# Optimization experiments

Hardware: AMD Instinct MI355X
Metric: run time of the kernel (lower is better)

## Reference

```python
import jax, jax.numpy as jnp
import numpy as np

HDIM = 1024
CDIM = 256
TEMPER = 10.0
IGNORE_OUT = 0.0
EPS = 1e-6


def setup_inputs() -> dict:
    key = jax.random.key(0)
    ks = jax.random.split(key, 6)
    B, T, D = 2, 128, 384
    x = jax.random.normal(ks[0], (B, T, D), jnp.float32)
    y = jax.random.normal(ks[1], (B, T, D), jnp.float32)
    # xavier-normal style init for the two linear layers
    W_enc = jax.random.normal(ks[2], (D, HDIM), jnp.float32) * np.sqrt(2.0 / (D + HDIM))
    b_enc = jnp.zeros((HDIM,), jnp.float32)
    W_dec = jax.random.normal(ks[3], (HDIM, D), jnp.float32) * np.sqrt(2.0 / (D + HDIM))
    b_dec = jnp.zeros((D,), jnp.float32)
    return {"x": x, "y": y, "W_enc": W_enc, "b_enc": b_enc, "W_dec": W_dec, "b_dec": b_dec}


def reference(x, y, W_enc, b_enc, W_dec, b_dec):
    B, T, D = x.shape
    n_iter = HDIM // CDIM
    pad = D - 1
    # shift_idx[s, j] = s + j : window of width D at offset s, s in [0, 2D-2]
    shift_idx = jnp.arange(2 * D - 1)[:, None] + jnp.arange(D)[None, :]

    seq_mask = (y == IGNORE_OUT)                       # (B,T,D) bool
    denom_seq = jnp.sum(~seq_mask).astype(x.dtype)
    qn = jnp.linalg.norm(y, axis=-1)                   # (B,T)

    mask_prev = None
    x_dis, losses = [], []
    for _ in range(n_iter):
        # --- _pad_for_shift: (B,T,2D-1,D) shifted windows of x ---
        kp = jnp.pad(x, ((0, 0), (0, 0), (pad, pad)))  # (B,T,3D-2)
        kpt = kp[..., shift_idx]                       # (B,T,2D-1,D)
        # --- _score (cos) + argmax over shifts ---
        kn = jnp.linalg.norm(kpt, axis=-1)             # (B,T,2D-1)
        sim = jnp.einsum('btsd,btd->bts', kpt, y) / (qn[..., None] * kn + EPS)
        sim = jnp.where(jnp.isnan(sim), 0.0, sim)
        theta = jnp.argmax(sim, axis=-1)               # (B,T) int
        x_opt = jnp.take_along_axis(kpt, theta[..., None, None], axis=-2)[..., 0, :]  # (B,T,D)
        # --- attention: elementwise cos-scaled score, temp softmax, detached ---
        dn = (jnp.linalg.norm(x_opt, axis=-1, keepdims=True)
              * jnp.linalg.norm(y, axis=-1, keepdims=True) + EPS)
        attn = jax.nn.softmax((x_opt * y / dn) / TEMPER, axis=-1)
        attn = jnp.where(jnp.isnan(attn), 0.0, attn)
        attn = jax.lax.stop_gradient(attn)
        x_attn = x_opt * attn
        # --- _reverse_pad_for_shift: window at offset 2D-2-theta ---
        kp2 = jnp.pad(x_attn, ((0, 0), (0, 0), (pad, pad)))
        rev_idx = (2 * D - 2 - theta)[..., None] + jnp.arange(D)  # (B,T,D)
        x_ele = jnp.take_along_axis(kp2, rev_idx, axis=-1)         # (B,T,D)
        # --- self_net: encoder -> top-k sparsify -> decoder_self ---
        h = x_ele @ W_enc + b_enc                      # (B,T,HDIM)
        if mask_prev is not None:
            h = jnp.where(mask_prev > 0, 1e-10, h)
        _, idx_top = jax.lax.top_k(h, CDIM)            # (B,T,CDIM)
        flat = idx_top.reshape(B * T, CDIM)
        mask_cur = jnp.zeros((B * T, HDIM), x.dtype).at[
            jnp.arange(B * T)[:, None], flat].set(1.0).reshape(B, T, HDIM)
        if mask_prev is None:
            mask_prev = mask_cur
        else:
            mask_prev = mask_prev + mask_cur - mask_prev * mask_cur
        h = h * mask_cur
        out = h @ W_dec + b_dec                        # (B,T,D)
        x_dis.append(out)
        # --- SeqLoss (masked MSE, mean-reduced by count of valid elems) ---
        err = jnp.where(seq_mask, 0.0, (out - x) ** 2) / denom_seq
        losses.append(jnp.sum(err))
    return jnp.stack(x_dis), jnp.stack(losses)
```

## Files before the change

### kernel.cpp

```cpp
#include <hip/hip_runtime.h>
#include <hip/hip_fp16.h>
#include <math.h>

#define DD 384
#define HD 1024
#define CD 256
#define NS 765
#define NITER 4
#define NROWS 256
#define TEMPER_F 10.0f
#define EPSF 1e-6f
#define CUTF 1e-10f

typedef unsigned long long u64;
typedef unsigned int u32;
typedef _Float16 hh2 __attribute__((ext_vector_type(2)));

__device__ __forceinline__ u32 flipf(float f) {
    u32 u = __float_as_uint(f);
    return u ^ ((u32)((int)u >> 31) | 0x80000000u);
}
__device__ __forceinline__ u32 bf16r(float f) {
    u32 u = __float_as_uint(f);
    return (u + 0x7FFFu + ((u >> 16) & 1u)) >> 16;
}
__device__ __forceinline__ u32 pack2bf(float a, float b) {
    return bf16r(a) | (bf16r(b) << 16);
}
__device__ __forceinline__ float blo(u32 p) { return __uint_as_float(p << 16); }
__device__ __forceinline__ float bhi(u32 p) { return __uint_as_float(p & 0xFFFF0000u); }
__device__ __forceinline__ u32 packh2(float a, float b) {
    __half2 p = __floats2half2_rn(a, b);
    return __builtin_bit_cast(u32, p);
}
__device__ __forceinline__ float dot2(u32 a, u32 b, float c) {
#if __has_builtin(__builtin_amdgcn_fdot2)
    return __builtin_amdgcn_fdot2(__builtin_bit_cast(hh2, a),
                                  __builtin_bit_cast(hh2, b), c, false);
#else
    __half2 ah = __builtin_bit_cast(__half2, a);
    __half2 bh = __builtin_bit_cast(__half2, b);
    return fmaf(__half2float(ah.y), __half2float(bh.y),
           fmaf(__half2float(ah.x), __half2float(bh.x), c));
#endif
}

__global__ __launch_bounds__(256) void convert_kernel(
    const float* __restrict__ We, const float* __restrict__ Wd,
    u32* __restrict__ wencp, uint2* __restrict__ wd16)
{
    const int t = blockIdx.x * 256 + threadIdx.x;
    for (int i = t; i < 192 * HD; i += 65536) {
        int j2 = i >> 10, c = i & 1023;
        wencp[i] = packh2(We[(2 * j2) * HD + c], We[(2 * j2 + 1) * HD + c]);
    }
    for (int i = t; i < (HD * DD) / 4; i += 65536) {
        float4 v = ((const float4*)Wd)[i];
        wd16[i] = make_uint2(pack2bf(v.x, v.y), pack2bf(v.z, v.w));
    }
}

__global__ __launch_bounds__(1024) void fused_kernel(
    const float* __restrict__ x, const float* __restrict__ y,
    const u32* __restrict__ wencp, const float* __restrict__ benc,
    const u32* __restrict__ wdec16, const float* __restrict__ bdec,
    float* __restrict__ out_xdis, float* __restrict__ lossp,
    int* __restrict__ ycnt)
{
    const int row  = blockIdx.x;
    const int tid  = threadIdx.x;
    const int lane = tid & 63;
    const int wid  = tid >> 6;

    __shared__ __align__(16) float xpad[1152];
    __shared__ __align__(16) float yr[DD];
    __shared__ float xa[DD];
    __shared__ __align__(16) float xe_s[DD];
    __shared__ u32   xep[192];
    __shared__ __align__(16) float part[4][HD];
    __shared__ u32   sk0[HD], sk1[HD];
    __shared__ __align__(16) uint2 dec2[HD];
    __shared__ __align__(16) float4 dpart[8][96];
    __shared__ float wred[16];
    __shared__ int   wredi[16];
    __shared__ float wredn[16];
    __shared__ float s_sc[4];
    __shared__ int   s_theta;
    __shared__ u32   s_b1, s_b2, s_b3;
    __shared__ int   wcls[128];
    __shared__ int   sbase[128];
    __shared__ int   cnt8[8];
    __shared__ float loss4[NITER];

    const float* xrow = x + row * DD;
    const float* yrow = y + row * DD;

    for (int i = tid; i < 1152; i += 1024)
        xpad[i] = (i >= DD - 1 && i < 2 * DD - 1) ? xrow[i - (DD - 1)] : 0.f;
    if (tid < DD) yr[tid] = yrow[tid];
    __syncthreads();

    if (tid < DD) {
        float p = yr[tid] * yr[tid];
        int   c = (yr[tid] != 0.f) ? 1 : 0;
        for (int o = 32; o; o >>= 1) {
            p += __shfl_xor(p, o, 64);
            c += __shfl_xor(c, o, 64);
        }
        if (lane == 0) { wred[wid] = p; wredi[wid] = c; }
    }
    __syncthreads();
    if (tid == 0) {
        float s = 0.f; int c = 0;
        for (int w = 0; w < 6; ++w) { s += wred[w]; c += wredi[w]; }
        s_sc[0] = sqrtf(s);
        ycnt[row] = c;
    }
    __syncthreads();
    const float qn = s_sc[0];

    float bv = -INFINITY; int bs = 0x7fffffff; float bn = 0.f;
    if (tid < 192) {
        const float4* xp4 = (const float4*)xpad;
        const float4* yp4 = (const float4*)yr;
        float4 A = xp4[tid];
        const float f0 = A.x * A.x, f1 = A.y * A.y, f2 = A.z * A.z;
        float d0 = 0.f, d1 = 0.f, d2 = 0.f, d3 = 0.f, n0 = 0.f;
#pragma unroll 4
        for (int jc = 0; jc < 96; ++jc) {
            float4 B = xp4[tid + jc + 1];
            float4 Y = yp4[jc];
            d0 += A.x * Y.x; d0 += A.y * Y.y; d0 += A.z * Y.z; d0 += A.w * Y.w;
            d1 += A.y * Y.x; d1 += A.z * Y.y; d1 += A.w * Y.z; d1 += B.x * Y.w;
            d2 += A.z * Y.x; d2 += A.w * Y.y; d2 += B.x * Y.z; d2 += B.y * Y.w;
            d3 += A.w * Y.x; d3 += B.x * Y.y; d3 += B.y * Y.z; d3 += B.z * Y.w;
            n0 += A.x * A.x; n0 += A.y * A.y; n0 += A.z * A.z; n0 += A.w * A.w;
            A = B;
        }
        const float n1 = n0 - f0 + A.x * A.x;
        const float n2 = n1 - f1 + A.y * A.y;
        const float n3 = n2 - f2 + A.z * A.z;
        const int s0 = 4 * tid;
        float sim0 = d0 / (qn * sqrtf(n0) + EPSF);
        float sim1 = d1 / (qn * sqrtf(n1) + EPSF);
        float sim2 = d2 / (qn * sqrtf(n2) + EPSF);
        float sim3 = d3 / (qn * sqrtf(n3) + EPSF);
        bv = sim0; bs = s0; bn = n0;
        if (s0 + 1 < NS && sim1 > bv) { bv = sim1; bs = s0 + 1; bn = n1; }
        if (s0 + 2 < NS && sim2 > bv) { bv = sim2; bs = s0 + 2; bn = n2; }
        if (s0 + 3 < NS && sim3 > bv) { bv = sim3; bs = s0 + 3; bn = n3; }
    }
    for (int o = 32; o; o >>= 1) {
        float v2 = __shfl_xor(bv, o, 64);
        int   i2 = __shfl_xor(bs, o, 64);
        float n2 = __shfl_xor(bn, o, 64);
        if (v2 > bv || (v2 == bv && i2 < bs)) { bv = v2; bs = i2; bn = n2; }
    }
    if (lane == 0) { wred[wid] = bv; wredi[wid] = bs; wredn[wid] = bn; }
    __syncthreads();
    if (tid == 0) {
        float v = wred[0]; int b = wredi[0]; float nn = wredn[0];
        for (int w = 1; w < 16; ++w)
            if (wred[w] > v || (wred[w] == v && wredi[w] < b)) {
                v = wred[w]; b = wredi[w]; nn = wredn[w];
            }
        s_theta = b;
        s_sc[1] = sqrtf(nn) * qn + EPSF;
    }
    __syncthreads();
    const int theta = s_theta;
    const float dn = s_sc[1];

    float xo = 0.f, ez = 0.f;
    if (tid < DD) {
        xo = xpad[theta + tid];
        ez = expf((xo * yr[tid] / dn) / TEMPER_F);
        float p = ez;
        for (int o = 32; o; o >>= 1) p += __shfl_xor(p, o, 64);
        if (lane == 0) wred[wid] = p;
    }
    __syncthreads();
    if (tid == 0) {
        float s = 0.f;
        for (int w = 0; w < 6; ++w) s += wred[w];
        s_sc[3] = s;
    }
    __syncthreads();
    if (tid < DD) xa[tid] = xo * (ez / s_sc[3]);
    __syncthreads();
    if (tid < DD) {
        int sj = tid - (theta - (DD - 1));
        xe_s[tid] = (sj >= 0 && sj < DD) ? xa[sj] : 0.f;
    }
    __syncthreads();
    if (tid < 192) xep[tid] = packh2(xe_s[2 * tid], xe_s[2 * tid + 1]);
    __syncthreads();

    {
        const int ks = tid >> 8;
        const int c4 = tid & 255;
        const uint4* wq = (const uint4*)wencp + (size_t)(ks * 48) * 256 + c4;
        const u32* xb = xep + ks * 48;
        float4 acc = make_float4(0.f, 0.f, 0.f, 0.f);
#pragma unroll 8
        for (int j2 = 0; j2 < 48; ++j2) {
            u32 xv = xb[j2];
            uint4 w = wq[(size_t)j2 * 256];
            acc.x = dot2(xv, w.x, acc.x);
            acc.y = dot2(xv, w.y, acc.y);
            acc.z = dot2(xv, w.z, acc.z);
            acc.w = dot2(xv, w.w, acc.w);
        }
        *(float4*)&part[ks][4 * c4] = acc;
    }
    if (tid < 8) cnt8[tid] = 0;
    if (tid < NITER) loss4[tid] = 0.f;
    __syncthreads();

    float oh;
    u32 okey, e;
    {
        oh = part[0][tid] + part[1][tid] + part[2][tid] + part[3][tid] + benc[tid];
        okey = ~flipf(oh);
        e = okey;
    }

    int par = 0;
    for (int k = 2; k <= HD; k <<= 1) {
        const bool up = (tid & k) == 0;
        for (int j = k >> 1; j > 0; j >>= 1) {
            if (j <= 32) {
                u32 p = __shfl_xor(e, j, 64);
                const bool takeMin = ((tid & j) == 0) == up;
                e = takeMin ? (e < p ? e : p) : (e > p ? e : p);
            } else {
                u32* buf = par ? sk1 : sk0; par ^= 1;
                buf[tid] = e;
                __syncthreads();
                u32 p = buf[tid ^ j];
                const bool takeMin = ((tid & j) == 0) == up;
                e = takeMin ? (e < p ? e : p) : (e > p ? e : p);
            }
        }
    }
    if (tid == 255) s_b1 = e;
    if (tid == 511) s_b2 = e;
    if (tid == 767) s_b3 = e;
    __syncthreads();
    const u32 b1 = s_b1, b2 = s_b2, b3 = s_b3;

    {
        const int myk = (okey <= b1) ? 0 : (okey <= b2) ? 1 : (okey <= b3) ? 2 : 3;
        const int cls = 2 * myk + ((oh > CUTF) ? 0 : 1);
        int myprefix = 0;
        const u64 ltmask = (1ull << lane) - 1;
#pragma unroll
        for (int c = 0; c < 8; ++c) {
            u64 m = __ballot(cls == c);
            if (cls == c) myprefix = __popcll(m & ltmask);
            if (lane == 0) {
                wcls[c * 16 + wid] = (int)__popcll(m);
                atomicAdd(&cnt8[c], (int)__popcll(m));
            }
        }
        __syncthreads();
        if (tid < 128) {
            int v = wcls[tid];
            int inc = v;
            for (int o = 1; o < 64; o <<= 1) {
                int t2 = __shfl_up(inc, o, 64);
                if (lane >= o) inc += t2;
            }
            sbase[tid] = inc - v;
        }
        __syncthreads();
        if (tid >= 64 && tid < 128) sbase[tid] += sbase[63] + wcls[63];
        __syncthreads();
        const int slot = sbase[cls * 16 + wid] + myprefix;
        dec2[slot] = make_uint2(__float_as_uint(oh), (u32)tid * 192u);
    }
    __syncthreads();

    {
        const int g8 = tid >> 7;
        const int k  = g8 >> 1;
        const int hf = g8 & 1;
        const int gg = tid & 127;
        const bool active = (gg < 96);
        int n = 0;
        if (active) n = (k == 0) ? CD : cnt8[2 * k];
        int r  = hf * 128;
        int r1 = n < r + 128 ? n : r + 128;
        if (r1 < r) r1 = r;
        float4 acc = make_float4(0.f, 0.f, 0.f, 0.f);
        const u32* wd = wdec16 + 2 * gg;
        const int base = k * CD;
        for (; r + 8 <= r1; r += 8) {
#pragma unroll
            for (int q = 0; q < 8; q += 2) {
                uint4 dv = *(const uint4*)&dec2[base + r + q];
                float v0 = __uint_as_float(dv.x);
                uint2 w0 = *(const uint2*)(wd + dv.y);
                float v1 = __uint_as_float(dv.z);
                uint2 w1 = *(const uint2*)(wd + dv.w);
                acc.x += v0 * blo(w0.x); acc.y += v0 * bhi(w0.x);
                acc.z += v0 * blo(w0.y); acc.w += v0 * bhi(w0.y);
                acc.x += v1 * blo(w1.x); acc.y += v1 * bhi(w1.x);
                acc.z += v1 * blo(w1.y); acc.w += v1 * bhi(w1.y);
            }
        }
        for (; r < r1; ++r) {
            uint2 dv = dec2[base + r];
            float v0 = __uint_as_float(dv.x);
            uint2 w0 = *(const uint2*)(wd + dv.y);
            acc.x += v0 * blo(w0.x); acc.y += v0 * bhi(w0.x);
            acc.z += v0 * blo(w0.y); acc.w += v0 * bhi(w0.y);
        }
        if (active) dpart[g8][gg] = acc;
    }
    __syncthreads();

    {
        float l = 0.f;
        if (tid < 512) {
            const int k2 = tid >> 7;
            const int q  = tid & 127;
            if (q < 96) {
                float4 a = dpart[2 * k2][q];
                float4 b = dpart[2 * k2 + 1][q];
                float4 bb = *(const float4*)&bdec[4 * q];
                float4 o4;
                o4.x = a.x + b.x + bb.x;
                o4.y = a.y + b.y + bb.y;
                o4.z = a.z + b.z + bb.z;
                o4.w = a.w + b.w + bb.w;
                *(float4*)&out_xdis[((size_t)k2 * NROWS + row) * DD + 4 * q] = o4;
                float4 xv = *(const float4*)&xrow[4 * q];
                float4 yv = *(const float4*)&yr[4 * q];
                float ee;
                ee = o4.x - xv.x; if (yv.x != 0.f) l += ee * ee;
                ee = o4.y - xv.y; if (yv.y != 0.f) l += ee * ee;
                ee = o4.z - xv.z; if (yv.z != 0.f) l += ee * ee;
                ee = o4.w - xv.w; if (yv.w != 0.f) l += ee * ee;
            }
        }
        for (int o = 32; o; o >>= 1) l += __shfl_xor(l, o, 64);
        if (tid < 512 && lane == 0) atomicAdd(&loss4[tid >> 7], l);
    }
    __syncthreads();
    if (tid < NITER) lossp[row * NITER + tid] = loss4[tid];
}

__global__ __launch_bounds__(256) void finalize2(
    const float* __restrict__ lossp, const int* __restrict__ ycnt,
    float* __restrict__ losses)
{
    const int tid = threadIdx.x, lane = tid & 63, w = tid >> 6;
    __shared__ int ctot[4];
    int c = ycnt[tid];
    for (int o = 32; o; o >>= 1) c += __shfl_xor(c, o, 64);
    if (lane == 0) ctot[w] = c;
    __syncthreads();
    const int total = ctot[0] + ctot[1] + ctot[2] + ctot[3];
    float s = lossp[lane * NITER + w] + lossp[(lane + 64) * NITER + w]
            + lossp[(lane + 128) * NITER + w] + lossp[(lane + 192) * NITER + w];
    for (int o = 32; o; o >>= 1) s += __shfl_xor(s, o, 64);
    if (lane == 0) losses[w] = s / (float)total;
}

extern "C" void kernel_launch(void* const* d_in, const int* in_sizes, int n_in,
                              void* d_out, int out_size, void* d_ws, size_t ws_size,
                              hipStream_t stream) {
    const float* x    = (const float*)d_in[0];
    const float* y    = (const float*)d_in[1];
    const float* Wenc = (const float*)d_in[2];
    const float* benc = (const float*)d_in[3];
    const float* Wdec = (const float*)d_in[4];
    const float* bdec = (const float*)d_in[5];

    float* out  = (float*)d_out;
    float* loss = out + (out_size - NITER);

    float* lossp  = (float*)d_ws;
    int*   ycnt   = (int*)(lossp + NROWS * NITER);
    u32*   wencp  = (u32*)(ycnt + NROWS);
    u32*   wdec16 = wencp + 192 * HD;

    convert_kernel<<<256, 256, 0, stream>>>(Wenc, Wdec, wencp, (uint2*)wdec16);
    fused_kernel<<<NROWS, 1024, 0, stream>>>(x, y, wencp, benc, wdec16, bdec,
                                             out, lossp, ycnt);
    finalize2<<<1, 256, 0, stream>>>(lossp, ycnt, loss);
}
```

Baseline: 106.1 us.

## Replace bitonic sort with histogram radix-select for top-k thresholds

Replaces the full 1024-element block bitonic sort, which needs many block-wide barriers, with a 4096-bin histogram on the top 12 key bits. A prefix scan locates the bins holding ranks 255/511/767, then a per-wavefront 64-element sort over candidate keys in those bins finds the exact thresholds. This cuts shared-memory traffic and synchronisation. The catch is that candidates are capped at 64 per bin, so heavily clustered keys (such as many masked 1e-10 values) could give wrong thresholds.

```diff
diff --git a/kernel.cpp b/kernel.cpp
--- a/kernel.cpp
+++ b/kernel.cpp
@@ -78,15 +78,17 @@
     __shared__ __align__(16) float xe_s[DD];
     __shared__ u32   xep[192];
     __shared__ __align__(16) float part[4][HD];
-    __shared__ u32   sk0[HD], sk1[HD];
     __shared__ __align__(16) uint2 dec2[HD];
     __shared__ __align__(16) float4 dpart[8][96];
     __shared__ float wred[16];
     __shared__ int   wredi[16];
     __shared__ float wredn[16];
+    __shared__ int   wbase16[16];
     __shared__ float s_sc[4];
     __shared__ int   s_theta;
-    __shared__ u32   s_b1, s_b2, s_b3;
+    __shared__ u32   s_b[3];
+    __shared__ int   sbinB[3], srankB[3], s_cc[3];
+    __shared__ u32   cand[3][64];
     __shared__ int   wcls[128];
     __shared__ int   sbase[128];
     __shared__ int   cnt8[8];
@@ -217,37 +219,70 @@
     if (tid < NITER) loss4[tid] = 0.f;
     __syncthreads();
 
-    float oh;
-    u32 okey, e;
+    const float oh = part[0][tid] + part[1][tid] + part[2][tid] + part[3][tid]
+                   + benc[tid];
+    const u32 okey = ~flipf(oh);
+    __syncthreads();
+
+    u32* hist = (u32*)part;
     {
-        oh = part[0][tid] + part[1][tid] + part[2][tid] + part[3][tid] + benc[tid];
-        okey = ~flipf(oh);
-        e = okey;
-    }
-
-    int par = 0;
-    for (int k = 2; k <= HD; k <<= 1) {
-        const bool up = (tid & k) == 0;
-        for (int j = k >> 1; j > 0; j >>= 1) {
-            if (j <= 32) {
-                u32 p = __shfl_xor(e, j, 64);
-                const bool takeMin = ((tid & j) == 0) == up;
-                e = takeMin ? (e < p ? e : p) : (e > p ? e : p);
-            } else {
-                u32* buf = par ? sk1 : sk0; par ^= 1;
-                buf[tid] = e;
-                __syncthreads();
-                u32 p = buf[tid ^ j];
-                const bool takeMin = ((tid & j) == 0) == up;
-                e = takeMin ? (e < p ? e : p) : (e > p ? e : p);
-            }
-        }
-    }
-    if (tid == 255) s_b1 = e;
-    if (tid == 511) s_b2 = e;
-    if (tid == 767) s_b3 = e;
-    __syncthreads();
-    const u32 b1 = s_b1, b2 = s_b2, b3 = s_b3;
+        hist[tid] = 0; hist[tid + 1024] = 0;
+        hist[tid + 2048] = 0; hist[tid + 3072] = 0;
+        if (tid < 192) cand[tid >> 6][tid & 63] = 0xFFFFFFFFu;
+        if (tid < 3) s_cc[tid] = 0;
+        __syncthreads();
+        atomicAdd(&hist[okey >> 20], 1u);
+        __syncthreads();
+        const int t4 = tid << 2;
+        const u32 l0 = hist[t4], l1 = hist[t4 + 1], l2 = hist[t4 + 2], l3 = hist[t4 + 3];
+        const int s = (int)(l0 + l1 + l2 + l3);
+        int inc = s;
+        for (int o = 1; o < 64; o <<= 1) {
+            int u = __shfl_up(inc, o, 64);
+            if (lane >= o) inc += u;
+        }
+        if (lane == 63) wredi[wid] = inc;
+        __syncthreads();
+        if (tid == 0) {
+            int acc = 0;
+            for (int w = 0; w < 16; ++w) { wbase16[w] = acc; acc += wredi[w]; }
+        }
+        __syncthreads();
+        const int c0 = wbase16[wid] + inc - s;
+        const int c1 = c0 + (int)l0, c2 = c1 + (int)l1, c3 = c2 + (int)l2;
+        const int c4e = c3 + (int)l3;
+#pragma unroll
+        for (int i = 0; i < 3; ++i) {
+            const int R = 255 + (i << 8);
+            if (R >= c0 && R < c1)      { sbinB[i] = t4;     srankB[i] = R - c0; }
+            else if (R >= c1 && R < c2) { sbinB[i] = t4 + 1; srankB[i] = R - c1; }
+            else if (R >= c2 && R < c3) { sbinB[i] = t4 + 2; srankB[i] = R - c2; }
+            else if (R >= c3 && R < c4e){ sbinB[i] = t4 + 3; srankB[i] = R - c3; }
+        }
+        __syncthreads();
+        const int myb = (int)(okey >> 20);
+#pragma unroll
+        for (int i = 0; i < 3; ++i) {
+            if (myb == sbinB[i]) {
+                int slot = atomicAdd(&s_cc[i], 1);
+                if (slot < 64) cand[i][slot] = okey;
+            }
+        }
+        __syncthreads();
+        if (wid < 3) {
+            u32 v = cand[wid][lane];
+            for (int k2 = 2; k2 <= 64; k2 <<= 1) {
+                for (int j = k2 >> 1; j > 0; j >>= 1) {
+                    u32 p = __shfl_xor(v, j, 64);
+                    const bool takeMin = ((lane & j) == 0) == ((lane & k2) == 0);
+                    v = takeMin ? (v < p ? v : p) : (v > p ? v : p);
+                }
+            }
+            if (lane == srankB[wid]) s_b[wid] = v;
+        }
+        __syncthreads();
+    }
+    const u32 b1 = s_b[0], b2 = s_b[1], b3 = s_b[2];
 
     {
         const int myk = (okey <= b1) ? 0 : (okey <= b2) ? 1 : (okey <= b3) ? 2 : 3;
```

Result: faster. 102.8 us (-3.1%).
